# Optimization experiments

Measured on AMD Instinct MI355X. Metric: run time of the kernel, lower is better.

The kernel has to match this reference:

```python
import jax, jax.numpy as jnp
import numpy as np

N, M, D = 8192, 8192, 256
EPS = 1e-7
NEG = -1e9


def setup_inputs() -> dict:
    key = jax.random.key(0)
    k1, k2, k3, k4 = jax.random.split(key, 4)
    xi = jax.random.normal(k1, (N, D), dtype=jnp.float32)
    xj = jax.random.normal(k2, (M, D), dtype=jnp.float32)
    # adjacency mask: random binary, int constant w.r.t. grads
    adj = jax.random.randint(k3, (N, M), 0, 2, dtype=jnp.int32)
    beta = jax.random.uniform(k4, (1,), dtype=jnp.float32)  # uniform(0,1) init
    return {"xi": xi, "xj": xj, "adj": adj, "beta": beta}


def reference(xi, xj, adj, beta):
    # row L2 norms -> outer product of norms (N, M)
    xi_n = jnp.linalg.norm(xi, axis=1, keepdims=True)        # (N, 1)
    xj_n = jnp.linalg.norm(xj, axis=1, keepdims=True).T      # (1, M)
    cos = beta * (xi @ xj.T) / (xi_n * xj_n + EPS)           # (N, M)
    mask = (1.0 - adj.astype(cos.dtype)) * NEG
    P = jax.nn.softmax(cos + mask, axis=1)                   # (N, M)
    return P @ xj                                            # (N, D)
```

## Files before the change

kernel.cpp:

```cpp
#include <hip/hip_runtime.h>
#include <hip/hip_bf16.h>


typedef _Float16 half8  __attribute__((ext_vector_type(8)));
typedef _Float16 half4v __attribute__((ext_vector_type(4)));
typedef __fp16   fp16x2 __attribute__((ext_vector_type(2)));
typedef float    f32x16 __attribute__((ext_vector_type(16)));
typedef int      i32x4  __attribute__((ext_vector_type(4)));
typedef unsigned long long u64;

#define GAS __attribute__((address_space(1)))
#define LAS __attribute__((address_space(3)))

#define N_ROWS 8192
#define M_ROWS 8192
#define DDIM   256

__global__ void prep_scale(const float* __restrict__ x, _Float16* __restrict__ xs,
                           const float* __restrict__ betap) {
    int row  = blockIdx.x * 4 + (threadIdx.x >> 6);
    int lane = threadIdx.x & 63;
    const float4 v = *(const float4*)(x + (size_t)row * DDIM + lane * 4);
    float ss = v.x * v.x + v.y * v.y + v.z * v.z + v.w * v.w;
#pragma unroll
    for (int o = 32; o > 0; o >>= 1) ss += __shfl_xor(ss, o, 64);
    float sc = betap[0] / sqrtf(ss);
    half4v hv = {(_Float16)(v.x * sc), (_Float16)(v.y * sc),
                 (_Float16)(v.z * sc), (_Float16)(v.w * sc)};
    *(half4v*)(xs + (size_t)row * DDIM + lane * 4) = hv;
}

__global__ void prep_xj(const float* __restrict__ xj, half8* __restrict__ xjA,
                        half8* __restrict__ xjF) {
    __shared__ _Float16 tileR[32][272];
    __shared__ _Float16 tileN[32][272];
    __shared__ float red[32][8];
    __shared__ float rsc[32];
    const int t  = threadIdx.x;
    const int jb = blockIdx.x;
    const int row = t >> 3, seg = t & 7;
    const float* src = xj + (size_t)(jb * 32 + row) * DDIM + seg * 32;
    float4 v[8];
    float ss = 0.f;
#pragma unroll
    for (int q = 0; q < 8; ++q) {
        v[q] = ((const float4*)src)[q];
        ss += v[q].x * v[q].x + v[q].y * v[q].y + v[q].z * v[q].z + v[q].w * v[q].w;
    }
    red[row][seg] = ss;
    __syncthreads();
    if (t < 32) {
        float s = 0.f;
#pragma unroll
        for (int q = 0; q < 8; ++q) s += red[t][q];
        rsc[t] = 1.0f / sqrtf(s);
    }
    __syncthreads();
    const float sc = rsc[row];
#pragma unroll
    for (int q = 0; q < 8; ++q) {
        int c = seg * 32 + q * 4;
        tileR[row][c + 0] = (_Float16)v[q].x;
        tileR[row][c + 1] = (_Float16)v[q].y;
        tileR[row][c + 2] = (_Float16)v[q].z;
        tileR[row][c + 3] = (_Float16)v[q].w;
        tileN[row][c + 0] = (_Float16)(v[q].x * sc);
        tileN[row][c + 1] = (_Float16)(v[q].y * sc);
        tileN[row][c + 2] = (_Float16)(v[q].z * sc);
        tileN[row][c + 3] = (_Float16)(v[q].w * sc);
    }
    __syncthreads();
#pragma unroll
    for (int rep = 0; rep < 4; ++rep) {
        int idx = t + rep * 256;
        int kt = idx >> 6, l = idx & 63, il = l & 31, hh = l >> 5;
        half8 val = *(const half8*)&tileN[il][kt * 16 + hh * 8];
        xjA[((size_t)jb * 16 + kt) * 64 + l] = val;
    }
#pragma unroll
    for (int rep = 0; rep < 4; ++rep) {
        int idx = t + rep * 256;
        int f = idx >> 7, s = (idx >> 6) & 1, l = idx & 63, il = l & 31, hh = l >> 5;
        int d = f * 32 + il, jl = s * 16 + hh * 8;
        half8 val;
#pragma unroll
        for (int e = 0; e < 8; ++e) val[e] = tileR[jl + e][d];
        xjF[((size_t)jb * 16 + f * 2 + s) * 64 + l] = val;
    }
}

__global__ void prep_mask(const int* __restrict__ adj, u64* __restrict__ maskW) {
    const int w    = threadIdx.x >> 6;
    const int lane = threadIdx.x & 63;
    const int task = blockIdx.x * 4 + w;
    const int row  = task >> 2;
    const int jq   = task & 3;
    const int* base = adj + (size_t)row * M_ROWS + jq * 2048 + lane * 4;
    i32x4 a[8];
#pragma unroll
    for (int k = 0; k < 8; ++k)
        a[k] = __builtin_nontemporal_load((const i32x4*)(base + k * 256));
    u64 myw = 0;
#pragma unroll
    for (int k = 0; k < 8; ++k) {
        u64 b0 = __ballot(a[k][0] != 0);
        u64 b1 = __ballot(a[k][1] != 0);
        u64 b2 = __ballot(a[k][2] != 0);
        u64 b3 = __ballot(a[k][3] != 0);
        if ((lane >> 2) == k) {
            int q = lane & 3;
            myw = (q == 0) ? b0 : (q == 1) ? b1 : (q == 2) ? b2 : b3;
        }
    }
    if (lane < 32)
        maskW[(size_t)row * 128 + jq * 32 + lane] = myw;
}

__global__ __launch_bounds__(256, 2)
void attn_main(const _Float16* __restrict__ xi_s, const half8* __restrict__ xjA,
               const half8* __restrict__ xjF, const u64* __restrict__ maskW,
               float* __restrict__ part, float* __restrict__ denp) {
    extern __shared__ char lds[];
    const int tid  = threadIdx.x;
    const int w    = tid >> 6;
    const int lane = tid & 63;
    const int il   = lane & 31;
    const int h    = lane >> 5;

    const int bid    = blockIdx.x;
    const int jsplit = bid & 7;
    const int itile  = bid >> 3;
    const int ibase  = itile * 128;
    const int irow   = ibase + w * 32 + il;
    const int j0blk  = jsplit * 32;

    half8 bq[16];
#pragma unroll
    for (int kt = 0; kt < 16; ++kt)
        bq[kt] = *(const half8*)(xi_s + (size_t)irow * DDIM + kt * 16 + h * 8);

    f32x16 acc[8];
#pragma unroll
    for (int f = 0; f < 8; ++f)
#pragma unroll
        for (int r = 0; r < 16; ++r) acc[f][r] = 0.f;
    float rden = 0.f;

    const u64* mrow = maskW + (size_t)irow * 128 + (jsplit >> 1) * 32;
    const int  kbase = (jsplit & 1) * 4;
    const char* gA = (const char*)xjA;
    const char* gF = (const char*)xjF;

#define STAGE(T, B)                                                             \
    {                                                                           \
        const size_t blk = (size_t)(j0blk + (T)) * 16384;                       \
        const char* src = (w < 2 ? gA : gF) + blk + (w & 1) * 8192 + (lane << 4); \
        char* dst = lds + (B) * 32768 + (w < 2 ? 0 : 16384) + (w & 1) * 8192 + (lane << 4); \
        _Pragma("unroll")                                                       \
        for (int k = 0; k < 8; ++k)                                             \
            __builtin_amdgcn_global_load_lds(                                   \
                (const GAS unsigned int*)(src + k * 1024),                      \
                (LAS unsigned int*)(dst + k * 1024), 16, 0, 0);                 \
    }

    STAGE(0, 0);
    u64 cw0, cw1, cw2, cw3;

    for (int t = 0; t < 32; ++t) {
        asm volatile("s_waitcnt vmcnt(0)" ::: "memory");
        __builtin_amdgcn_s_barrier();
        __builtin_amdgcn_sched_barrier(0);

        if ((t & 7) == 0) {
            int k = kbase + (t >> 3);
            cw0 = mrow[k * 4 + 0]; cw1 = mrow[k * 4 + 1];
            cw2 = mrow[k * 4 + 2]; cw3 = mrow[k * 4 + 3];
        }
        if (t < 31) STAGE(t + 1, (t + 1) & 1);

        const char* bufA = lds + (t & 1) * 32768;
        const char* bufF = bufA + 16384;

        f32x16 sacc0, sacc1;
#pragma unroll
        for (int r = 0; r < 16; ++r) { sacc0[r] = 0.f; sacc1[r] = 0.f; }
#pragma unroll
        for (int kt = 0; kt < 16; kt += 2) {
            half8 a0 = *(const half8*)(bufA + kt * 1024 + (lane << 4));
            sacc0 = __builtin_amdgcn_mfma_f32_32x32x16_f16(a0, bq[kt], sacc0, 0, 0, 0);
            half8 a1 = *(const half8*)(bufA + (kt + 1) * 1024 + (lane << 4));
            sacc1 = __builtin_amdgcn_mfma_f32_32x32x16_f16(a1, bq[kt + 1], sacc1, 0, 0, 0);
        }
        const unsigned s0 = 8 * (t & 7) + h;
        unsigned x0 = (unsigned)(cw0 >> s0), x1 = (unsigned)(cw1 >> s0);
        unsigned x2 = (unsigned)(cw2 >> s0), x3 = (unsigned)(cw3 >> s0);
        float wv[16];
#pragma unroll
        for (int r = 0; r < 16; ++r) {
            unsigned xq = (r & 3) == 0 ? x0 : (r & 3) == 1 ? x1 : (r & 3) == 2 ? x2 : x3;
            float e = ((xq >> (2 * (r >> 2))) & 1u) ? __expf(sacc0[r] + sacc1[r]) : 0.f;
            wv[r] = e;
            rden += e;
        }
        int pq[8], qq[8];
#pragma unroll
        for (int q = 0; q < 8; ++q) {
            fp16x2 pp = __builtin_amdgcn_cvt_pkrtz(wv[2 * q], wv[2 * q + 1]);
            pq[q] = __builtin_bit_cast(int, pp);
            qq[q] = __shfl_xor(pq[q], 32, 64);
        }
        i32x4 af0 = {h ? qq[2] : pq[0], h ? qq[3] : pq[1], h ? pq[2] : qq[0], h ? pq[3] : qq[1]};
        i32x4 af1 = {h ? qq[6] : pq[4], h ? qq[7] : pq[5], h ? pq[6] : qq[4], h ? pq[7] : qq[5]};
        half8 afA = __builtin_bit_cast(half8, af0);
        half8 afB = __builtin_bit_cast(half8, af1);

#pragma unroll
        for (int f = 0; f < 8; ++f) {
            half8 b0 = *(const half8*)(bufF + (f * 2 + 0) * 1024 + (lane << 4));
            acc[f] = __builtin_amdgcn_mfma_f32_32x32x16_f16(afA, b0, acc[f], 0, 0, 0);
            half8 b1 = *(const half8*)(bufF + (f * 2 + 1) * 1024 + (lane << 4));
            acc[f] = __builtin_amdgcn_mfma_f32_32x32x16_f16(afB, b1, acc[f], 0, 0, 0);
        }
    }

    rden += __shfl_xor(rden, 32, 64);
    if (lane < 32) denp[(size_t)jsplit * N_ROWS + ibase + w * 32 + lane] = rden;

    float* prow = part + (size_t)jsplit * ((size_t)N_ROWS * DDIM);
#pragma unroll
    for (int f = 0; f < 8; ++f) {
#pragma unroll
        for (int r = 0; r < 16; ++r) {
            int ir = (r & 3) + 8 * (r >> 2) + 4 * h;
            prow[(size_t)(ibase + w * 32 + ir) * DDIM + f * 32 + il] = acc[f][r];
        }
    }
#undef STAGE
}

__global__ void reduce_out(const float* __restrict__ part, const float* __restrict__ denp,
                           float* __restrict__ out) {
    const int row = blockIdx.x;
    const int d   = threadIdx.x;
    float s = 0.f;
#pragma unroll
    for (int q = 0; q < 8; ++q)
        s += part[((size_t)q * N_ROWS + row) * DDIM + d];
    float dn = 0.f;
#pragma unroll
    for (int q = 0; q < 8; ++q)
        dn += denp[(size_t)q * N_ROWS + row];
    out[(size_t)row * DDIM + d] = s / dn;
}

extern "C" void kernel_launch(void* const* d_in, const int* in_sizes, int n_in,
                              void* d_out, int out_size, void* d_ws, size_t ws_size,
                              hipStream_t stream) {
    const float* xi   = (const float*)d_in[0];
    const float* xj   = (const float*)d_in[1];
    const int*   adj  = (const int*)d_in[2];
    const float* beta = (const float*)d_in[3];
    float* out = (float*)d_out;
    char*  ws  = (char*)d_ws;

    _Float16* xi_s  = (_Float16*)(ws);
    half8*    xjA   = (half8*)(ws + (4u << 20));
    half8*    xjF   = (half8*)(ws + (8u << 20));
    float*    denp  = (float*)(ws + (12u << 20));
    u64*      maskW = (u64*)(ws + (13u << 20));
    float*    part  = (float*)(ws + (24u << 20));

    hipFuncSetAttribute((const void*)attn_main,
                        hipFuncAttributeMaxDynamicSharedMemorySize, 65536);

    prep_scale<<<N_ROWS / 4, 256, 0, stream>>>(xi, xi_s, beta);
    prep_xj<<<M_ROWS / 32, 256, 0, stream>>>(xj, xjA, xjF);
    prep_mask<<<N_ROWS * 4 / 4, 256, 0, stream>>>(adj, maskW);
    attn_main<<<512, 256, 65536, stream>>>(xi_s, xjA, xjF, maskW, part, denp);
    reduce_out<<<N_ROWS, 256, 0, stream>>>(part, denp, out);
}
```

Baseline: 154.3 us.

## Fuse adjacency bitmask packing into attention kernel with software-pipelined loads

Removes the separate prep_mask kernel and its bitmask round trip through the workspace. The attention kernel now reads the int32 adjacency rows directly and packs them with wave ballots. Loads for the next 256-column chunk are issued alongside the LDS staging and converted after the MFMA work, so memory latency overlaps compute. The cost is extra VGPRs for the in-flight loads and a vmcnt(0) wait that now also covers the adjacency loads, which may stall the pipeline. The 256 MB adjacency read is still needed either way.

```diff
diff --git a/kernel.cpp b/kernel.cpp
--- a/kernel.cpp
+++ b/kernel.cpp
@@ -89,36 +89,9 @@
     }
 }
 
-__global__ void prep_mask(const int* __restrict__ adj, u64* __restrict__ maskW) {
-    const int w    = threadIdx.x >> 6;
-    const int lane = threadIdx.x & 63;
-    const int task = blockIdx.x * 4 + w;
-    const int row  = task >> 2;
-    const int jq   = task & 3;
-    const int* base = adj + (size_t)row * M_ROWS + jq * 2048 + lane * 4;
-    i32x4 a[8];
-#pragma unroll
-    for (int k = 0; k < 8; ++k)
-        a[k] = __builtin_nontemporal_load((const i32x4*)(base + k * 256));
-    u64 myw = 0;
-#pragma unroll
-    for (int k = 0; k < 8; ++k) {
-        u64 b0 = __ballot(a[k][0] != 0);
-        u64 b1 = __ballot(a[k][1] != 0);
-        u64 b2 = __ballot(a[k][2] != 0);
-        u64 b3 = __ballot(a[k][3] != 0);
-        if ((lane >> 2) == k) {
-            int q = lane & 3;
-            myw = (q == 0) ? b0 : (q == 1) ? b1 : (q == 2) ? b2 : b3;
-        }
-    }
-    if (lane < 32)
-        maskW[(size_t)row * 128 + jq * 32 + lane] = myw;
-}
-
 __global__ __launch_bounds__(256, 2)
 void attn_main(const _Float16* __restrict__ xi_s, const half8* __restrict__ xjA,
-               const half8* __restrict__ xjF, const u64* __restrict__ maskW,
+               const half8* __restrict__ xjF, const int* __restrict__ adj,
                float* __restrict__ part, float* __restrict__ denp) {
     extern __shared__ char lds[];
     const int tid  = threadIdx.x;
@@ -146,10 +119,9 @@
         for (int r = 0; r < 16; ++r) acc[f][r] = 0.f;
     float rden = 0.f;
 
-    const u64* mrow = maskW + (size_t)irow * 128 + (jsplit >> 1) * 32;
-    const int  kbase = (jsplit & 1) * 4;
     const char* gA = (const char*)xjA;
     const char* gF = (const char*)xjF;
+    const int* arow0 = adj + (size_t)(ibase + w * 32) * M_ROWS + jsplit * 1024 + 4 * lane;
 
 #define STAGE(T, B)                                                             \
     {                                                                           \
@@ -164,17 +136,31 @@
     }
 
     STAGE(0, 0);
-    u64 cw0, cw1, cw2, cw3;
+
+    u64 cw0 = 0, cw1 = 0, cw2 = 0, cw3 = 0;
+    u64 nw0 = 0, nw1 = 0, nw2 = 0, nw3 = 0;
+#pragma unroll 4
+    for (int riw = 0; riw < 32; ++riw) {
+        i32x4 av = __builtin_nontemporal_load((const i32x4*)(arow0 + (size_t)riw * M_ROWS));
+        u64 b0 = __ballot(av[0] != 0);
+        u64 b1 = __ballot(av[1] != 0);
+        u64 b2 = __ballot(av[2] != 0);
+        u64 b3 = __ballot(av[3] != 0);
+        if (il == riw) { cw0 = b0; cw1 = b1; cw2 = b2; cw3 = b3; }
+    }
 
     for (int t = 0; t < 32; ++t) {
         asm volatile("s_waitcnt vmcnt(0)" ::: "memory");
         __builtin_amdgcn_s_barrier();
         __builtin_amdgcn_sched_barrier(0);
 
-        if ((t & 7) == 0) {
-            int k = kbase + (t >> 3);
-            cw0 = mrow[k * 4 + 0]; cw1 = mrow[k * 4 + 1];
-            cw2 = mrow[k * 4 + 2]; cw3 = mrow[k * 4 + 3];
+        i32x4 av[4];
+        const int r0 = 4 * (t & 7);
+        if (t < 24) {
+            const int* ap = arow0 + ((t >> 3) + 1) * 256 + (size_t)r0 * M_ROWS;
+#pragma unroll
+            for (int rr = 0; rr < 4; ++rr)
+                av[rr] = __builtin_nontemporal_load((const i32x4*)(ap + (size_t)rr * M_ROWS));
         }
         if (t < 31) STAGE(t + 1, (t + 1) & 1);
 
@@ -221,6 +207,18 @@
             half8 b1 = *(const half8*)(bufF + (f * 2 + 1) * 1024 + (lane << 4));
             acc[f] = __builtin_amdgcn_mfma_f32_32x32x16_f16(afB, b1, acc[f], 0, 0, 0);
         }
+
+        if (t < 24) {
+#pragma unroll
+            for (int rr = 0; rr < 4; ++rr) {
+                u64 b0 = __ballot(av[rr][0] != 0);
+                u64 b1 = __ballot(av[rr][1] != 0);
+                u64 b2 = __ballot(av[rr][2] != 0);
+                u64 b3 = __ballot(av[rr][3] != 0);
+                if (il == r0 + rr) { nw0 = b0; nw1 = b1; nw2 = b2; nw3 = b3; }
+            }
+        }
+        if ((t & 7) == 7) { cw0 = nw0; cw1 = nw1; cw2 = nw2; cw3 = nw3; }
     }
 
     rden += __shfl_xor(rden, 32, 64);
@@ -267,7 +265,6 @@
     half8*    xjA   = (half8*)(ws + (4u << 20));
     half8*    xjF   = (half8*)(ws + (8u << 20));
     float*    denp  = (float*)(ws + (12u << 20));
-    u64*      maskW = (u64*)(ws + (13u << 20));
     float*    part  = (float*)(ws + (24u << 20));
 
     hipFuncSetAttribute((const void*)attn_main,
@@ -275,7 +272,6 @@
 
     prep_scale<<<N_ROWS / 4, 256, 0, stream>>>(xi, xi_s, beta);
     prep_xj<<<M_ROWS / 32, 256, 0, stream>>>(xj, xjA, xjF);
-    prep_mask<<<N_ROWS * 4 / 4, 256, 0, stream>>>(adj, maskW);
-    attn_main<<<512, 256, 65536, stream>>>(xi_s, xjA, xjF, maskW, part, denp);
+    attn_main<<<512, 256, 65536, stream>>>(xi_s, xjA, xjF, adj, part, denp);
     reduce_out<<<N_ROWS, 256, 0, stream>>>(part, denp, out);
 }
```

Result: slower. 175.1 us (+13.5%).
